# Kernel optimization log

Hardware: AMD Instinct MI355X
Metric: run time of the kernel (lower is better)

## Reference

```python
import jax, jax.numpy as jnp
import numpy as np

N = 200000
CIN = 64
COUT = 64
K = 9           # taps in a 1x3x3 or 3x1x3 kernel
EPS = 1e-5      # BatchNorm1d eps
SLOPE = 0.01    # LeakyReLU default negative slope


def setup_inputs() -> dict:
    key = jax.random.key(0)
    ks = jax.random.split(key, 7)
    scale = 0.05
    return {
        "x": jax.random.normal(ks[0], (N, CIN), dtype=jnp.float32),
        "w_a0": jax.random.normal(ks[1], (K, CIN, COUT), dtype=jnp.float32) * scale,
        "gamma_a0": jnp.ones((COUT,), jnp.float32),
        "beta_a0": jnp.zeros((COUT,), jnp.float32),
        "w_a1": jax.random.normal(ks[2], (K, COUT, COUT), dtype=jnp.float32) * scale,
        "gamma_a1": jnp.ones((COUT,), jnp.float32),
        "beta_a1": jnp.zeros((COUT,), jnp.float32),
        "w_b0": jax.random.normal(ks[3], (K, CIN, COUT), dtype=jnp.float32) * scale,
        "gamma_b0": jnp.ones((COUT,), jnp.float32),
        "beta_b0": jnp.zeros((COUT,), jnp.float32),
        "w_b1": jax.random.normal(ks[4], (K, COUT, COUT), dtype=jnp.float32) * scale,
        "gamma_b1": jnp.ones((COUT,), jnp.float32),
        "beta_b1": jnp.zeros((COUT,), jnp.float32),
        "idx_133": jax.random.randint(ks[5], (N, K), 0, N),
        "idx_313": jax.random.randint(ks[6], (N, K), 0, N),
    }


def subm_conv(feat, idx, w):
    # gather [N,K,Cin] -> GEMM with [K,Cin,Cout] -> [N,Cout]
    gathered = feat[idx]
    return jnp.einsum('nkc,kcd->nd', gathered, w)


def bn_train(feat, gamma, beta):
    # BatchNorm1d (training mode): biased batch statistics over N
    mean = jnp.mean(feat, axis=0)
    var = jnp.var(feat, axis=0)
    return (feat - mean) * jax.lax.rsqrt(var + EPS) * gamma + beta


def lrelu(feat):
    return jnp.where(feat >= 0, feat, SLOPE * feat)


def reference(x, w_a0, gamma_a0, beta_a0, w_a1, gamma_a1, beta_a1,
              w_b0, gamma_b0, beta_b0, w_b1, gamma_b1, beta_b1,
              idx_133, idx_313):
    # A branch: 1x3x3 -> act -> bn -> 3x1x3 -> act -> bn
    A = subm_conv(x, idx_133, w_a0)
    A = bn_train(lrelu(A), gamma_a0, beta_a0)
    A = subm_conv(A, idx_313, w_a1)
    A = bn_train(lrelu(A), gamma_a1, beta_a1)
    # B0 branch is computed but unused in the original (B = conv_B1(A))
    B0 = bn_train(lrelu(subm_conv(x, idx_313, w_b0)), gamma_b0, beta_b0)  # noqa: F841 (dead, DCE'd)
    # B branch actually uses A per original source
    B = subm_conv(A, idx_133, w_b1)
    B = bn_train(lrelu(B), gamma_b1, beta_b1)
    return A + B
```

## Files before the change

kernel.cpp:

```cpp
#include <hip/hip_runtime.h>

#define N_ROWS 200000
#define CH 64
#define NTAP 9
#define BM 128
#define NBLK 1563
#define WT_PER_CONV (64*576)
#define TAB_ELEMS ((size_t)N_ROWS*CH)
#define VEC8_CNT 1600000

using bf16x8 = __attribute__((ext_vector_type(8))) __bf16;
using f32x4  = __attribute__((ext_vector_type(4))) float;

__device__ __forceinline__ float b2f(unsigned short u) {
  unsigned int x = ((unsigned int)u) << 16;
  return __builtin_bit_cast(float, x);
}
__device__ __forceinline__ unsigned short f2b(float f) {
  unsigned int x = __builtin_bit_cast(unsigned int, f);
  x = x + 0x7fffu + ((x >> 16) & 1u);
  return (unsigned short)(x >> 16);
}

__global__ void prep_w(const float* __restrict__ wa, const float* __restrict__ wb,
                       const float* __restrict__ wc, unsigned short* __restrict__ wt) {
  int i = blockIdx.x * 256 + threadIdx.x;
  if (i >= 3 * WT_PER_CONV) return;
  int conv = i / WT_PER_CONV, r = i % WT_PER_CONV;
  int n = r / 576, k = r % 576;
  int tap = k >> 6, ci = k & 63;
  const float* w = conv == 0 ? wa : (conv == 1 ? wb : wc);
  wt[i] = f2b(w[tap * 4096 + ci * 64 + n]);
}

__global__ void prep_x(const float* __restrict__ x, unsigned short* __restrict__ T) {
  int i = blockIdx.x * 256 + threadIdx.x;
  if (i >= VEC8_CNT) return;
  const float4* xv = (const float4*)x + (size_t)i * 2;
  float4 a = xv[0], b = xv[1];
  uint4 o;
  o.x = (unsigned)f2b(a.x) | ((unsigned)f2b(a.y) << 16);
  o.y = (unsigned)f2b(a.z) | ((unsigned)f2b(a.w) << 16);
  o.z = (unsigned)f2b(b.x) | ((unsigned)f2b(b.y) << 16);
  o.w = (unsigned)f2b(b.z) | ((unsigned)f2b(b.w) << 16);
  ((uint4*)T)[i] = o;
}

__global__ __launch_bounds__(512, 4) void conv_k(
    const unsigned short* __restrict__ T,
    const int* __restrict__ idx,
    const unsigned short* __restrict__ Wt,
    unsigned short* __restrict__ Yout,
    float* __restrict__ partials)
{
  __shared__ unsigned short Wlds[64][584];
  __shared__ float psum[8][2][64];

  const int tid = threadIdx.x;
  const int w = tid >> 6;
  const int l = tid & 63;
  const int blk = blockIdx.x;
  const int rowbase = blk * BM;
  const int kgrp = l >> 4;

  int mrow = rowbase + w * 16 + (l & 15);
  if (mrow > N_ROWS - 1) mrow = N_ROWS - 1;

  unsigned off[NTAP];
#pragma unroll
  for (int t = 0; t < NTAP; ++t)
    off[t] = (unsigned)idx[mrow * NTAP + t] * 128u + (unsigned)(kgrp * 16);

  const char* Tb = (const char*)T;
  bf16x8 A0[NTAP], A1[NTAP];
#pragma unroll
  for (int t = 0; t < NTAP; ++t) {
    A0[t] = *(const bf16x8*)(Tb + off[t]);
    A1[t] = *(const bf16x8*)(Tb + off[t] + 64);
  }

  for (int v = tid; v < 64 * 72; v += 512) {
    int n = v / 72, k0 = (v % 72) * 8;
    uint4 d = *reinterpret_cast<const uint4*>(Wt + n * 576 + k0);
    *reinterpret_cast<uint4*>(&Wlds[n][k0]) = d;
  }
  __syncthreads();

  f32x4 acc[4] = {};
#pragma unroll
  for (int t = 0; t < NTAP; ++t) {
    const unsigned short* wb = &Wlds[l & 15][t * 64 + kgrp * 8];
#pragma unroll
    for (int f = 0; f < 4; ++f) {
      bf16x8 b0 = *(const bf16x8*)(wb + f * 16 * 584);
      bf16x8 b1 = *(const bf16x8*)(wb + f * 16 * 584 + 32);
      acc[f] = __builtin_amdgcn_mfma_f32_16x16x32_bf16(A0[t], b0, acc[f], 0, 0, 0);
      acc[f] = __builtin_amdgcn_mfma_f32_16x16x32_bf16(A1[t], b1, acc[f], 0, 0, 0);
    }
  }

#pragma unroll
  for (int f = 0; f < 4; ++f) {
    int c = f * 16 + (l & 15);
    float sm = 0.f, sq = 0.f;
#pragma unroll
    for (int j = 0; j < 4; ++j) {
      int gr = rowbase + w * 16 + kgrp * 4 + j;
      float v = acc[f][j];
      float y = v >= 0.f ? v : 0.01f * v;
      if (gr < N_ROWS) {
        Yout[(size_t)gr * 64 + c] = f2b(y);
        sm += y; sq += y * y;
      }
    }
    sm += __shfl_xor(sm, 16); sm += __shfl_xor(sm, 32);
    sq += __shfl_xor(sq, 16); sq += __shfl_xor(sq, 32);
    if (l < 16) { psum[w][0][c] = sm; psum[w][1][c] = sq; }
  }
  __syncthreads();
  if (tid < 128) {
    int j = tid >> 6, c = tid & 63;
    float tot = 0.f;
#pragma unroll
    for (int ww = 0; ww < 8; ++ww) tot += psum[ww][j][c];
    partials[(size_t)(j * 64 + c) * NBLK + blk] = tot;
  }
}

__global__ void reduce_k(const float* __restrict__ part, const float* __restrict__ gamma,
                         const float* __restrict__ beta, float* __restrict__ stats) {
  int c = blockIdx.x, t = threadIdx.x;
  float s = 0.f, q = 0.f;
  for (int b = t; b < NBLK; b += 256) {
    s += part[(size_t)c * NBLK + b];
    q += part[(size_t)(64 + c) * NBLK + b];
  }
#pragma unroll
  for (int m = 1; m < 64; m <<= 1) { s += __shfl_xor(s, m); q += __shfl_xor(q, m); }
  __shared__ float rs[4], rq[4];
  if ((t & 63) == 0) { rs[t >> 6] = s; rq[t >> 6] = q; }
  __syncthreads();
  if (t == 0) {
    float su = rs[0] + rs[1] + rs[2] + rs[3];
    float qu = rq[0] + rq[1] + rq[2] + rq[3];
    float mean = su / (float)N_ROWS;
    float var = qu / (float)N_ROWS - mean * mean;
    float r = rsqrtf(var + 1e-5f);
    float sc = gamma[c] * r;
    stats[c] = sc;
    stats[64 + c] = beta[c] - mean * sc;
  }
}

__global__ void transform_k(const unsigned short* __restrict__ Y,
                            const float* __restrict__ stats,
                            unsigned short* __restrict__ T) {
  int i = blockIdx.x * 256 + threadIdx.x;
  if (i >= VEC8_CNT) return;
  uint4 yv = ((const uint4*)Y)[i];
  int c0 = (i & 7) * 8;
  const float* S = stats + c0;
  const float* B = stats + 64 + c0;
  unsigned v[4] = {yv.x, yv.y, yv.z, yv.w};
  unsigned ov[4];
#pragma unroll
  for (int h = 0; h < 4; ++h) {
    float y0 = b2f((unsigned short)(v[h] & 0xffff));
    float y1 = b2f((unsigned short)(v[h] >> 16));
    y0 = y0 >= 0.f ? y0 : 0.01f * y0;
    y1 = y1 >= 0.f ? y1 : 0.01f * y1;
    float o0 = y0 * S[2 * h] + B[2 * h];
    float o1 = y1 * S[2 * h + 1] + B[2 * h + 1];
    ov[h] = (unsigned)f2b(o0) | ((unsigned)f2b(o1) << 16);
  }
  uint4 o; o.x = ov[0]; o.y = ov[1]; o.z = ov[2]; o.w = ov[3];
  ((uint4*)T)[i] = o;
}

__global__ void final_k(const unsigned short* __restrict__ A,
                        const unsigned short* __restrict__ Y,
                        const float* __restrict__ stats, float* __restrict__ out) {
  int i = blockIdx.x * 256 + threadIdx.x;
  if (i >= VEC8_CNT) return;
  uint4 av = ((const uint4*)A)[i];
  uint4 yv = ((const uint4*)Y)[i];
  int c0 = (i & 7) * 8;
  const float* S = stats + c0;
  const float* B = stats + 64 + c0;
  unsigned va[4] = {av.x, av.y, av.z, av.w};
  unsigned vy[4] = {yv.x, yv.y, yv.z, yv.w};
  float o[8];
#pragma unroll
  for (int h = 0; h < 4; ++h) {
    float a0 = b2f((unsigned short)(va[h] & 0xffff));
    float a1 = b2f((unsigned short)(va[h] >> 16));
    float y0 = b2f((unsigned short)(vy[h] & 0xffff));
    float y1 = b2f((unsigned short)(vy[h] >> 16));
    y0 = y0 >= 0.f ? y0 : 0.01f * y0;
    y1 = y1 >= 0.f ? y1 : 0.01f * y1;
    o[2 * h]     = a0 + y0 * S[2 * h]     + B[2 * h];
    o[2 * h + 1] = a1 + y1 * S[2 * h + 1] + B[2 * h + 1];
  }
  float4* ov = (float4*)(out + (size_t)i * 8);
  ov[0] = make_float4(o[0], o[1], o[2], o[3]);
  ov[1] = make_float4(o[4], o[5], o[6], o[7]);
}

extern "C" void kernel_launch(void* const* d_in, const int* in_sizes, int n_in,
                              void* d_out, int out_size, void* d_ws, size_t ws_size,
                              hipStream_t stream) {
  (void)in_sizes; (void)n_in; (void)out_size; (void)ws_size;
  const float* x    = (const float*)d_in[0];
  const float* w_a0 = (const float*)d_in[1];
  const float* g_a0 = (const float*)d_in[2];
  const float* b_a0 = (const float*)d_in[3];
  const float* w_a1 = (const float*)d_in[4];
  const float* g_a1 = (const float*)d_in[5];
  const float* b_a1 = (const float*)d_in[6];
  const float* w_b1 = (const float*)d_in[10];
  const float* g_b1 = (const float*)d_in[11];
  const float* b_b1 = (const float*)d_in[12];
  const int* idx133 = (const int*)d_in[13];
  const int* idx313 = (const int*)d_in[14];
  float* out = (float*)d_out;

  char* ws = (char*)d_ws;
  unsigned short* wt = (unsigned short*)ws;
  unsigned short* Ta = (unsigned short*)(ws + 221184);
  unsigned short* Tb = Ta + TAB_ELEMS;
  unsigned short* Yb = Tb + TAB_ELEMS;
  float* part = (float*)(ws + 221184 + 3 * 2 * TAB_ELEMS);
  float* st1 = part + 2 * 64 * NBLK;
  float* st2 = st1 + 128;
  float* st3 = st2 + 128;

  prep_w<<<(3 * WT_PER_CONV + 255) / 256, 256, 0, stream>>>(w_a0, w_a1, w_b1, wt);
  prep_x<<<(VEC8_CNT + 255) / 256, 256, 0, stream>>>(x, Ta);

  conv_k<<<NBLK, 512, 0, stream>>>(Ta, idx133, wt, Yb, part);
  reduce_k<<<64, 256, 0, stream>>>(part, g_a0, b_a0, st1);
  transform_k<<<(VEC8_CNT + 255) / 256, 256, 0, stream>>>(Yb, st1, Ta);

  conv_k<<<NBLK, 512, 0, stream>>>(Ta, idx313, wt + WT_PER_CONV, Yb, part);
  reduce_k<<<64, 256, 0, stream>>>(part, g_a1, b_a1, st2);
  transform_k<<<(VEC8_CNT + 255) / 256, 256, 0, stream>>>(Yb, st2, Tb);

  conv_k<<<NBLK, 512, 0, stream>>>(Tb, idx133, wt + 2 * WT_PER_CONV, Yb, part);
  reduce_k<<<64, 256, 0, stream>>>(part, g_b1, b_b1, st3);

  final_k<<<(VEC8_CNT + 255) / 256, 256, 0, stream>>>(Tb, Yb, st3, out);
}
```

Baseline: 254.4 us.

## Fold BatchNorm affine into next conv weights and bias, drop transform passes

BatchNorm scale is folded into the next conv's bf16 weights, and the shift becomes a per-output bias. This removes the two full-tensor transform kernels, and the final kernel applies both BN affines directly. The gather indices are also transposed to tap-major layout so per-tap index loads coalesce. Weights are staged into LDS with async global_load_lds, issued before the gathers. The cost is extra small prep kernels plus index transposes on every call, and folding scale into bf16 weights changes rounding.

New measurement: 220.3 us. 1.15x faster.

```diff
diff --git a/kernel.cpp b/kernel.cpp
--- a/kernel.cpp
+++ b/kernel.cpp
@@ -1,12 +1,13 @@
 #include <hip/hip_runtime.h>
 
 #define N_ROWS 200000
-#define CH 64
 #define NTAP 9
 #define BM 128
 #define NBLK 1563
-#define WT_PER_CONV (64*576)
-#define TAB_ELEMS ((size_t)N_ROWS*CH)
+#define WSTRIDE 584
+#define WCHUNKS 73
+#define WT_ELEMS (64*WSTRIDE)
+#define TAB_ELEMS ((size_t)N_ROWS*64)
 #define VEC8_CNT 1600000
 
 using bf16x8 = __attribute__((ext_vector_type(8))) __bf16;
@@ -21,16 +22,17 @@
   x = x + 0x7fffu + ((x >> 16) & 1u);
   return (unsigned short)(x >> 16);
 }
-
-__global__ void prep_w(const float* __restrict__ wa, const float* __restrict__ wb,
-                       const float* __restrict__ wc, unsigned short* __restrict__ wt) {
-  int i = blockIdx.x * 256 + threadIdx.x;
-  if (i >= 3 * WT_PER_CONV) return;
-  int conv = i / WT_PER_CONV, r = i % WT_PER_CONV;
-  int n = r / 576, k = r % 576;
-  int tap = k >> 6, ci = k & 63;
-  const float* w = conv == 0 ? wa : (conv == 1 ? wb : wc);
-  wt[i] = f2b(w[tap * 4096 + ci * 64 + n]);
+__device__ __forceinline__ void async16(const void* g, void* l) {
+  __builtin_amdgcn_global_load_lds((const __attribute__((address_space(1))) unsigned int*)g,
+                                   (__attribute__((address_space(3))) unsigned int*)l,
+                                   16, 0, 0);
+}
+
+__global__ void transp_idx(const int* __restrict__ src, int* __restrict__ dst) {
+  int i = blockIdx.x * 256 + threadIdx.x;
+  if (i >= N_ROWS * NTAP) return;
+  int n = i / NTAP, t = i - n * NTAP;
+  dst[t * N_ROWS + n] = src[i];
 }
 
 __global__ void prep_x(const float* __restrict__ x, unsigned short* __restrict__ T) {
@@ -46,14 +48,44 @@
   ((uint4*)T)[i] = o;
 }
 
+__global__ void prep_ws(const float* __restrict__ w, const float* __restrict__ stats,
+                        unsigned short* __restrict__ wt) {
+  int i = blockIdx.x * 256 + threadIdx.x;
+  if (i >= WT_ELEMS) return;
+  int n = i / WSTRIDE, k = i - n * WSTRIDE;
+  float v = 0.f;
+  if (k < 576) {
+    int tap = k >> 6, ci = k & 63;
+    float s = stats ? stats[ci] : 1.0f;
+    v = w[tap * 4096 + ci * 64 + n] * s;
+  }
+  wt[i] = f2b(v);
+}
+
+__global__ void prep_bias(const float* __restrict__ w, const float* __restrict__ stats,
+                          float* __restrict__ bias) {
+  int co = threadIdx.x & 63, part = threadIdx.x >> 6;
+  float s = 0.f;
+#pragma unroll 4
+  for (int e = part; e < 576; e += 4) {
+    int tap = e >> 6, ci = e & 63;
+    s += stats[64 + ci] * w[tap * 4096 + ci * 64 + co];
+  }
+  __shared__ float r[4][64];
+  r[part][co] = s;
+  __syncthreads();
+  if (part == 0) bias[co] = r[0][co] + r[1][co] + r[2][co] + r[3][co];
+}
+
 __global__ __launch_bounds__(512, 4) void conv_k(
     const unsigned short* __restrict__ T,
-    const int* __restrict__ idx,
+    const int* __restrict__ idxT,
     const unsigned short* __restrict__ Wt,
-    unsigned short* __restrict__ Yout,
+    const float* __restrict__ bias,
+    unsigned short* __restrict__ L,
     float* __restrict__ partials)
 {
-  __shared__ unsigned short Wlds[64][584];
+  __shared__ unsigned short Wlds[64][WSTRIDE];
   __shared__ float psum[8][2][64];
 
   const int tid = threadIdx.x;
@@ -63,37 +95,45 @@
   const int rowbase = blk * BM;
   const int kgrp = l >> 4;
 
+  for (int c = w; c < WCHUNKS; c += 8)
+    async16(Wt + c * 512 + l * 8, (unsigned short*)&Wlds[0][0] + c * 512);
+
   int mrow = rowbase + w * 16 + (l & 15);
   if (mrow > N_ROWS - 1) mrow = N_ROWS - 1;
 
-  unsigned off[NTAP];
-#pragma unroll
-  for (int t = 0; t < NTAP; ++t)
-    off[t] = (unsigned)idx[mrow * NTAP + t] * 128u + (unsigned)(kgrp * 16);
+  int ix[NTAP];
+#pragma unroll
+  for (int t = 0; t < NTAP; ++t) ix[t] = idxT[t * N_ROWS + mrow];
+
+  float binit[4] = {0.f, 0.f, 0.f, 0.f};
+  if (bias) {
+#pragma unroll
+    for (int f = 0; f < 4; ++f) binit[f] = bias[f * 16 + (l & 15)];
+  }
+
+  __syncthreads();
 
   const char* Tb = (const char*)T;
   bf16x8 A0[NTAP], A1[NTAP];
 #pragma unroll
   for (int t = 0; t < NTAP; ++t) {
-    A0[t] = *(const bf16x8*)(Tb + off[t]);
-    A1[t] = *(const bf16x8*)(Tb + off[t] + 64);
-  }
-
-  for (int v = tid; v < 64 * 72; v += 512) {
-    int n = v / 72, k0 = (v % 72) * 8;
-    uint4 d = *reinterpret_cast<const uint4*>(Wt + n * 576 + k0);
-    *reinterpret_cast<uint4*>(&Wlds[n][k0]) = d;
-  }
-  __syncthreads();
-
-  f32x4 acc[4] = {};
+    const char* p = Tb + (size_t)((unsigned)ix[t] * 128u) + kgrp * 16;
+    A0[t] = *(const bf16x8*)p;
+    A1[t] = *(const bf16x8*)(p + 64);
+  }
+  __builtin_amdgcn_sched_barrier(0);
+
+  f32x4 acc[4];
+#pragma unroll
+  for (int f = 0; f < 4; ++f) acc[f] = (f32x4){binit[f], binit[f], binit[f], binit[f]};
+
 #pragma unroll
   for (int t = 0; t < NTAP; ++t) {
     const unsigned short* wb = &Wlds[l & 15][t * 64 + kgrp * 8];
 #pragma unroll
     for (int f = 0; f < 4; ++f) {
-      bf16x8 b0 = *(const bf16x8*)(wb + f * 16 * 584);
-      bf16x8 b1 = *(const bf16x8*)(wb + f * 16 * 584 + 32);
+      bf16x8 b0 = *(const bf16x8*)(wb + f * 16 * WSTRIDE);
+      bf16x8 b1 = *(const bf16x8*)(wb + f * 16 * WSTRIDE + 32);
       acc[f] = __builtin_amdgcn_mfma_f32_16x16x32_bf16(A0[t], b0, acc[f], 0, 0, 0);
       acc[f] = __builtin_amdgcn_mfma_f32_16x16x32_bf16(A1[t], b1, acc[f], 0, 0, 0);
     }
@@ -109,7 +149,7 @@
       float v = acc[f][j];
       float y = v >= 0.f ? v : 0.01f * v;
       if (gr < N_ROWS) {
-        Yout[(size_t)gr * 64 + c] = f2b(y);
+        L[(size_t)gr * 64 + c] = f2b(y);
         sm += y; sq += y * y;
       }
     }
@@ -152,54 +192,27 @@
   }
 }
 
-__global__ void transform_k(const unsigned short* __restrict__ Y,
-                            const float* __restrict__ stats,
-                            unsigned short* __restrict__ T) {
+__global__ void final_k(const unsigned short* __restrict__ L2v,
+                        const unsigned short* __restrict__ L3v,
+                        const float* __restrict__ st2, const float* __restrict__ st3,
+                        float* __restrict__ out) {
   int i = blockIdx.x * 256 + threadIdx.x;
   if (i >= VEC8_CNT) return;
-  uint4 yv = ((const uint4*)Y)[i];
+  uint4 av = ((const uint4*)L2v)[i];
+  uint4 yv = ((const uint4*)L3v)[i];
   int c0 = (i & 7) * 8;
-  const float* S = stats + c0;
-  const float* B = stats + 64 + c0;
-  unsigned v[4] = {yv.x, yv.y, yv.z, yv.w};
-  unsigned ov[4];
-#pragma unroll
-  for (int h = 0; h < 4; ++h) {
-    float y0 = b2f((unsigned short)(v[h] & 0xffff));
-    float y1 = b2f((unsigned short)(v[h] >> 16));
-    y0 = y0 >= 0.f ? y0 : 0.01f * y0;
-    y1 = y1 >= 0.f ? y1 : 0.01f * y1;
-    float o0 = y0 * S[2 * h] + B[2 * h];
-    float o1 = y1 * S[2 * h + 1] + B[2 * h + 1];
-    ov[h] = (unsigned)f2b(o0) | ((unsigned)f2b(o1) << 16);
-  }
-  uint4 o; o.x = ov[0]; o.y = ov[1]; o.z = ov[2]; o.w = ov[3];
-  ((uint4*)T)[i] = o;
-}
-
-__global__ void final_k(const unsigned short* __restrict__ A,
-                        const unsigned short* __restrict__ Y,
-                        const float* __restrict__ stats, float* __restrict__ out) {
-  int i = blockIdx.x * 256 + threadIdx.x;
-  if (i >= VEC8_CNT) return;
-  uint4 av = ((const uint4*)A)[i];
-  uint4 yv = ((const uint4*)Y)[i];
-  int c0 = (i & 7) * 8;
-  const float* S = stats + c0;
-  const float* B = stats + 64 + c0;
   unsigned va[4] = {av.x, av.y, av.z, av.w};
   unsigned vy[4] = {yv.x, yv.y, yv.z, yv.w};
   float o[8];
 #pragma unroll
   for (int h = 0; h < 4; ++h) {
+    int c = c0 + 2 * h;
     float a0 = b2f((unsigned short)(va[h] & 0xffff));
     float a1 = b2f((unsigned short)(va[h] >> 16));
     float y0 = b2f((unsigned short)(vy[h] & 0xffff));
     float y1 = b2f((unsigned short)(vy[h] >> 16));
-    y0 = y0 >= 0.f ? y0 : 0.01f * y0;
-    y1 = y1 >= 0.f ? y1 : 0.01f * y1;
-    o[2 * h]     = a0 + y0 * S[2 * h]     + B[2 * h];
-    o[2 * h + 1] = a1 + y1 * S[2 * h + 1] + B[2 * h + 1];
+    o[2 * h]     = a0 * st2[c]     + st2[64 + c]     + y0 * st3[c]     + st3[64 + c];
+    o[2 * h + 1] = a1 * st2[c + 1] + st2[64 + c + 1] + y1 * st3[c + 1] + st3[64 + c + 1];
   }
   float4* ov = (float4*)(out + (size_t)i * 8);
   ov[0] = make_float4(o[0], o[1], o[2], o[3]);
@@ -225,28 +238,39 @@
   float* out = (float*)d_out;
 
   char* ws = (char*)d_ws;
-  unsigned short* wt = (unsigned short*)ws;
-  unsigned short* Ta = (unsigned short*)(ws + 221184);
-  unsigned short* Tb = Ta + TAB_ELEMS;
-  unsigned short* Yb = Tb + TAB_ELEMS;
-  float* part = (float*)(ws + 221184 + 3 * 2 * TAB_ELEMS);
+  unsigned short* wt0 = (unsigned short*)ws;
+  unsigned short* wt1 = wt0 + WT_ELEMS;
+  unsigned short* wt2 = wt1 + WT_ELEMS;
+  unsigned short* Tx  = wt2 + WT_ELEMS;
+  unsigned short* L1  = Tx + TAB_ELEMS;
+  unsigned short* L2  = L1 + TAB_ELEMS;
+  unsigned short* L3  = Tx;
+  int* it133 = (int*)(L2 + TAB_ELEMS);
+  int* it313 = it133 + N_ROWS * NTAP;
+  float* part = (float*)(it313 + N_ROWS * NTAP);
   float* st1 = part + 2 * 64 * NBLK;
   float* st2 = st1 + 128;
   float* st3 = st2 + 128;
-
-  prep_w<<<(3 * WT_PER_CONV + 255) / 256, 256, 0, stream>>>(w_a0, w_a1, w_b1, wt);
-  prep_x<<<(VEC8_CNT + 255) / 256, 256, 0, stream>>>(x, Ta);
-
-  conv_k<<<NBLK, 512, 0, stream>>>(Ta, idx133, wt, Yb, part);
+  float* bias1 = st3 + 128;
+  float* bias2 = bias1 + 64;
+
+  transp_idx<<<(N_ROWS * NTAP + 255) / 256, 256, 0, stream>>>(idx133, it133);
+  transp_idx<<<(N_ROWS * NTAP + 255) / 256, 256, 0, stream>>>(idx313, it313);
+  prep_x<<<(VEC8_CNT + 255) / 256, 256, 0, stream>>>(x, Tx);
+  prep_ws<<<(WT_ELEMS + 255) / 256, 256, 0, stream>>>(w_a0, nullptr, wt0);
+
+  conv_k<<<NBLK, 512, 0, stream>>>(Tx, it133, wt0, nullptr, L1, part);
   reduce_k<<<64, 256, 0, stream>>>(part, g_a0, b_a0, st1);
-  transform_k<<<(VEC8_CNT + 255) / 256, 256, 0, stream>>>(Yb, st1, Ta);
-
-  conv_k<<<NBLK, 512, 0, stream>>>(Ta, idx313, wt + WT_PER_CONV, Yb, part);
+  prep_ws<<<(WT_ELEMS + 255) / 256, 256, 0, stream>>>(w_a1, st1, wt1);
+  prep_bias<<<1, 256, 0, stream>>>(w_a1, st1, bias1);
+
+  conv_k<<<NBLK, 512, 0, stream>>>(L1, it313, wt1, bias1, L2, part);
   reduce_k<<<64, 256, 0, stream>>>(part, g_a1, b_a1, st2);
-  transform_k<<<(VEC8_CNT + 255) / 256, 256, 0, stream>>>(Yb, st2, Tb);
-
-  conv_k<<<NBLK, 512, 0, stream>>>(Tb, idx133, wt + 2 * WT_PER_CONV, Yb, part);
+  prep_ws<<<(WT_ELEMS + 255) / 256, 256, 0, stream>>>(w_b1, st2, wt2);
+  prep_bias<<<1, 256, 0, stream>>>(w_b1, st2, bias2);
+
+  conv_k<<<NBLK, 512, 0, stream>>>(L2, it133, wt2, bias2, L3, part);
   reduce_k<<<64, 256, 0, stream>>>(part, g_b1, b_b1, st3);
 
-  final_k<<<(VEC8_CNT + 255) / 256, 256, 0, stream>>>(Tb, Yb, st3, out);
-}
+  final_k<<<(VEC8_CNT + 255) / 256, 256, 0, stream>>>(L2, L3, st2, st3, out);
+}
```
